# Kernel optimization log

Hardware: AMD Instinct MI355X
Metric: run time of the kernel (lower is better)

The kernel has to match this reference:

```python
import jax, jax.numpy as jnp
import numpy as np

N = 30000        # nodes
E = 480000       # edges
IN_DIM = 128
HID = 64
OUT = 64
POS_DIM = 32
H = 4            # heads (same for all layers)
PVOCAB = 3
NEG_SLOPE = 0.2


def _xavier(key, shape):
    fan_in, fan_out = shape[0], shape[-1] if len(shape) > 1 else shape[0]
    scale = 1.414 * np.sqrt(2.0 / (fan_in + fan_out))
    return jax.random.normal(key, shape, dtype=jnp.float32) * scale


def setup_inputs() -> dict:
    key = jax.random.key(0)
    ks = jax.random.split(key, 20)
    d0_in = IN_DIM + POS_DIM            # 160
    d_mid = HID * H + POS_DIM           # 288
    inp = {
        "features": jax.random.normal(ks[0], (N, IN_DIM), dtype=jnp.float32),
        # layer 0
        "W0": _xavier(ks[1], (d0_in, H * HID)),
        "al0": _xavier(ks[2], (H, HID)),
        "ar0": _xavier(ks[3], (H, HID)),
        "pe0": _xavier(ks[4], (PVOCAB, POS_DIM)),
        # layer 1
        "W1": _xavier(ks[5], (d_mid, H * HID)),
        "al1": _xavier(ks[6], (H, HID)),
        "ar1": _xavier(ks[7], (H, HID)),
        "pe1": _xavier(ks[8], (PVOCAB, POS_DIM)),
        # output layer
        "W2": _xavier(ks[9], (d_mid, H * OUT)),
        "al2": _xavier(ks[10], (H, OUT)),
        "ar2": _xavier(ks[11], (H, OUT)),
        "pe2": _xavier(ks[12], (PVOCAB, POS_DIM)),
        # graph
        "src": jax.random.randint(ks[13], (E,), 0, N, dtype=jnp.int32),
        "dst": jax.random.randint(ks[14], (E,), 0, N, dtype=jnp.int32),
        "pos": jax.random.randint(ks[15], (N,), 0, PVOCAB, dtype=jnp.int32),
    }
    return inp


def gat_layer(h, W, a_l, a_r, src, dst):
    # h: [N, in_d]; W: [in_d, H*d]; a_l,a_r: [H, d]
    n = h.shape[0]
    nh, d = a_l.shape
    ft = (h @ W).reshape(n, nh, d)                       # [N,H,d]
    a1 = jnp.einsum("nhd,hd->nh", ft, a_l)               # [N,H]
    a2 = jnp.einsum("nhd,hd->nh", ft, a_r)               # [N,H]
    e = jax.nn.leaky_relu(a1[src] + a2[dst], NEG_SLOPE)  # [E,H]
    # per-destination segment softmax (numerically stable)
    m = jax.ops.segment_max(e, dst, num_segments=n)      # [N,H]
    ex = jnp.exp(e - m[dst])                             # [E,H]
    s = jax.ops.segment_sum(ex, dst, num_segments=n)     # [N,H]
    alpha = ex / s[dst]                                  # [E,H]
    msg = ft[src] * alpha[:, :, None]                    # [E,H,d]
    return jax.ops.segment_sum(msg, dst, num_segments=n) # [N,H,d]


def reference(features, W0, al0, ar0, pe0, W1, al1, ar1, pe1,
              W2, al2, ar2, pe2, src, dst, pos):
    h = features
    # hidden GAT layers with ELU activation and head-flattening
    for W, al, ar, pe in ((W0, al0, ar0, pe0), (W1, al1, ar1, pe1)):
        p = pe[pos]                                      # [N, pos_dim]
        hcat = jnp.concatenate((h, p), axis=1)
        out = gat_layer(hcat, W, al, ar, src, dst)       # [N,H,d]
        h = jax.nn.elu(out.reshape(out.shape[0], -1))    # [N,H*d]
    # output layer: mean over heads
    p = pe2[pos]
    hcat = jnp.concatenate((h, p), axis=1)
    out = gat_layer(hcat, W2, al2, ar2, src, dst)        # [N,H,out]
    return out.mean(axis=1)                              # [N,out]
```

## Files before the change

### kernel.cpp

```cpp
#include <hip/hip_runtime.h>
#include <hip/hip_fp16.h>
#include <math.h>

#define N_NODES 30000
#define N_EDGES 480000
#define HEADS 4
#define DHEAD 64
#define FDIM 256
#define POSD 32
#define CAPB 96
#define HIST_NB 1875
#define G0_NB 940

typedef _Float16 half8 __attribute__((ext_vector_type(8)));
typedef float floatx4 __attribute__((ext_vector_type(4)));

__device__ __forceinline__ float lrelu(float x){ return x > 0.f ? x : 0.2f * x; }

template<typename T>
__device__ __forceinline__ void gemm_body(
    int bx, int by, const T* __restrict__ A, const _Float16* __restrict__ Wt,
    const float* __restrict__ PW, const int* __restrict__ pos,
    const float* __restrict__ al, const float* __restrict__ arw,
    _Float16* __restrict__ Ch, float* __restrict__ a1, float* __restrict__ a2,
    int K){
  int t = threadIdx.x;
  int w = t >> 6;
  int lane = t & 63;
  int lm = lane & 15;
  int kq = lane >> 4;
  int h = bx;
  int rowBase = by * 128 + w * 32;
  int colBase = h * DHEAD;

  floatx4 acc[2][4] = {};

  const T* Ar[2];
#pragma unroll
  for (int r = 0; r < 2; r++)
    Ar[r] = A + (size_t)min(rowBase + r * 16 + lm, N_NODES - 1) * K;
  const _Float16* Bp[4];
#pragma unroll
  for (int j = 0; j < 4; j++)
    Bp[j] = Wt + (size_t)(colBase + j * 16 + lm) * K;

  for (int kb = 0; kb < K; kb += 32){
    int ko = kb + kq * 8;
    half8 bf[4];
#pragma unroll
    for (int j = 0; j < 4; j++) bf[j] = *(const half8*)(Bp[j] + ko);
#pragma unroll
    for (int r = 0; r < 2; r++){
      half8 af;
      if constexpr (sizeof(T) == 2){
        af = *(const half8*)(Ar[r] + ko);
      } else {
        float4 u0 = *(const float4*)(Ar[r] + ko);
        float4 u1 = *(const float4*)(Ar[r] + ko + 4);
        af[0] = (_Float16)u0.x; af[1] = (_Float16)u0.y;
        af[2] = (_Float16)u0.z; af[3] = (_Float16)u0.w;
        af[4] = (_Float16)u1.x; af[5] = (_Float16)u1.y;
        af[6] = (_Float16)u1.z; af[7] = (_Float16)u1.w;
      }
#pragma unroll
      for (int j = 0; j < 4; j++)
        acc[r][j] = __builtin_amdgcn_mfma_f32_16x16x32_f16(af, bf[j], acc[r][j], 0, 0, 0);
    }
  }

  float alw[4], arr[4];
#pragma unroll
  for (int j = 0; j < 4; j++){
    int col = j * 16 + lm;
    alw[j] = al [h * DHEAD + col];
    arr[j] = arw[h * DHEAD + col];
  }

#pragma unroll
  for (int r = 0; r < 2; r++){
#pragma unroll
    for (int p = 0; p < 4; p++){
      int row = rowBase + r * 16 + kq * 4 + p;
      if (row >= N_NODES) continue;
      int pz = pos[row];
      const float* pwb = PW + pz * FDIM + colBase;
      float s1 = 0.f, s2 = 0.f;
#pragma unroll
      for (int j = 0; j < 4; j++){
        float v = acc[r][j][p] + pwb[j * 16 + lm];
        Ch[(size_t)row * FDIM + colBase + j * 16 + lm] = (_Float16)v;
        s1 = fmaf(v, alw[j], s1);
        s2 = fmaf(v, arr[j], s2);
      }
#pragma unroll
      for (int o2 = 1; o2 <= 8; o2 <<= 1){
        s1 += __shfl_xor(s1, o2, 64);
        s2 += __shfl_xor(s2, o2, 64);
      }
      if (lm == 0){
        a1[row * HEADS + h] = s1;
        a2[row * HEADS + h] = s2;
      }
    }
  }
}

template<typename T>
__global__ __launch_bounds__(256, 2) void gemm_k(
    const T* __restrict__ A, const _Float16* __restrict__ Wt,
    const float* __restrict__ PW, const int* __restrict__ pos,
    const float* __restrict__ al, const float* __restrict__ arw,
    _Float16* __restrict__ Ch, float* __restrict__ a1, float* __restrict__ a2,
    int K){
  gemm_body<T>(blockIdx.x, blockIdx.y, A, Wt, PW, pos, al, arw, Ch, a1, a2, K);
}

__global__ __launch_bounds__(256) void prep0_k(
    const float* __restrict__ W0, const float* __restrict__ pe0,
    _Float16* __restrict__ T0, float* __restrict__ PW,
    int* __restrict__ deg){
  int blk = blockIdx.x;
  int n = threadIdx.x;
  if (blk < 64){
    for (int k = blk; k < 128; k += 64)
      T0[(size_t)n * 128 + k] = (_Float16)W0[(size_t)k * FDIM + n];
  } else if (blk < 67){
    int v = blk - 64;
    float s = 0.f;
#pragma unroll
    for (int k = 0; k < POSD; k++)
      s = fmaf(pe0[v * POSD + k], W0[(size_t)(128 + k) * FDIM + n], s);
    PW[v * FDIM + n] = s;
  } else {
    int i = (blk - 67) * 256 + n;
    if (i < N_NODES) deg[i] = 0;
  }
}

__global__ __launch_bounds__(256, 2) void fused0_k(
    const float* __restrict__ A, const _Float16* __restrict__ Wt0,
    const float* __restrict__ PW0, const int* __restrict__ pos,
    const float* __restrict__ al0, const float* __restrict__ ar0,
    _Float16* __restrict__ Ch, float* __restrict__ a1, float* __restrict__ a2,
    const int* __restrict__ src, const int* __restrict__ dst,
    int* __restrict__ deg, int* __restrict__ esrc,
    const float* __restrict__ W1, const float* __restrict__ W2,
    _Float16* __restrict__ T1, _Float16* __restrict__ T2,
    const float* __restrict__ pe1, const float* __restrict__ pe2,
    float* __restrict__ PWall){
  int blk = blockIdx.x;
  if (blk < G0_NB){
    gemm_body<float>(blk & 3, blk >> 2, A, Wt0, PW0, pos, al0, ar0,
                     Ch, a1, a2, 128);
  } else if (blk < G0_NB + HIST_NB){
    int e = (blk - G0_NB) * 256 + threadIdx.x;
    if (e < N_EDGES){
      int d = dst[e];
      int slot = atomicAdd(&deg[d], 1);
      if (slot < CAPB) esrc[d * CAPB + slot] = src[e];
    }
  } else if (blk < G0_NB + HIST_NB + 128){
    int q = blk - G0_NB - HIST_NB;
    int l = q >> 6, kk0 = q & 63;
    const float* W = l == 0 ? W1 : W2;
    _Float16* T    = l == 0 ? T1 : T2;
    int n = threadIdx.x;
    for (int k = kk0; k < 256; k += 64)
      T[(size_t)n * 256 + k] = (_Float16)W[(size_t)k * FDIM + n];
  } else {
    int q = blk - G0_NB - HIST_NB - 128;
    int layer = q / 3 + 1, v = q % 3;
    const float* W  = layer == 1 ? W1 : W2;
    const float* pe = layer == 1 ? pe1 : pe2;
    int j = threadIdx.x;
    float s = 0.f;
#pragma unroll
    for (int k = 0; k < POSD; k++)
      s = fmaf(pe[v * POSD + k], W[(size_t)(256 + k) * FDIM + j], s);
    PWall[(layer * 3 + v) * FDIM + j] = s;
  }
}

__global__ __launch_bounds__(256) void agg4_k(
    const _Float16* __restrict__ ft, const float* __restrict__ a1,
    const float* __restrict__ a2, const int* __restrict__ degv,
    const int* __restrict__ esrc, _Float16* __restrict__ outh,
    float* __restrict__ outf, int mode){
  int wv = threadIdx.x >> 6;
  int lane = threadIdx.x & 63;
  int n = blockIdx.x * 4 + wv;
  if (n >= N_NODES) return;
  int jb = n * CAPB;
  int deg = min(degv[n], CAPB);
  int eidx = lane & 15, h = lane >> 4;
  int hsel = h << 4;
  float a2n = a2[n * HEADS + h];
  float4 acc = make_float4(0.f, 0.f, 0.f, 0.f);
  const _Float16* ftl = ft + lane * 4;
  struct h4 { __half2 a, b; };

  if (deg <= 64){
    int sreg[4]; float wreg[4];
    float m = -INFINITY;
#pragma unroll
    for (int r = 0; r < 4; r++){
      int idx = eidx + r * 16;
      int s = (idx < deg) ? esrc[jb + idx] : 0;
      sreg[r] = s;
      float e = (idx < deg) ? lrelu(a1[s * HEADS + h] + a2n) : -INFINITY;
      wreg[r] = e;
      m = fmaxf(m, e);
    }
    m = fmaxf(m, __shfl_xor(m, 1, 64));
    m = fmaxf(m, __shfl_xor(m, 2, 64));
    m = fmaxf(m, __shfl_xor(m, 4, 64));
    m = fmaxf(m, __shfl_xor(m, 8, 64));
    float ss = 0.f;
#pragma unroll
    for (int r = 0; r < 4; r++){
      int idx = eidx + r * 16;
      float tv = (idx < deg) ? __expf(wreg[r] - m) : 0.f;
      wreg[r] = tv;
      ss += tv;
    }
    ss += __shfl_xor(ss, 1, 64);
    ss += __shfl_xor(ss, 2, 64);
    ss += __shfl_xor(ss, 4, 64);
    ss += __shfl_xor(ss, 8, 64);
    float inv = (ss > 0.f) ? 1.f / ss : 0.f;
#pragma unroll
    for (int r = 0; r < 4; r++) wreg[r] *= inv;

#pragma unroll
    for (int r = 0; r < 4; r++){
      if (r * 16 >= deg) break;
      int lim = deg - r * 16; if (lim > 16) lim = 16;
      float wr = wreg[r]; int sr = sreg[r];
      int jj = 0;
      for (; jj + 8 <= lim; jj += 8){
        float w8[8]; int s8[8]; h4 f8[8];
#pragma unroll
        for (int u = 0; u < 8; u++){
          w8[u] = __shfl(wr, (jj + u) | hsel, 64);
          s8[u] = __shfl(sr, jj + u, 64);
        }
#pragma unroll
        for (int u = 0; u < 8; u++)
          f8[u] = *(const h4*)(ftl + (size_t)s8[u] * FDIM);
#pragma unroll
        for (int u = 0; u < 8; u++){
          float2 fa = __half22float2(f8[u].a), fb = __half22float2(f8[u].b);
          acc.x = fmaf(w8[u], fa.x, acc.x);
          acc.y = fmaf(w8[u], fa.y, acc.y);
          acc.z = fmaf(w8[u], fb.x, acc.z);
          acc.w = fmaf(w8[u], fb.y, acc.w);
        }
      }
      for (; jj < lim; jj += 4){
        float w4[4]; int s4[4]; h4 f4[4];
#pragma unroll
        for (int u = 0; u < 4; u++){
          w4[u] = __shfl(wr, (jj + u) | hsel, 64);
          s4[u] = __shfl(sr, jj + u, 64);
        }
#pragma unroll
        for (int u = 0; u < 4; u++)
          f4[u] = *(const h4*)(ftl + (size_t)s4[u] * FDIM);
#pragma unroll
        for (int u = 0; u < 4; u++){
          float2 fa = __half22float2(f4[u].a), fb = __half22float2(f4[u].b);
          acc.x = fmaf(w4[u], fa.x, acc.x);
          acc.y = fmaf(w4[u], fa.y, acc.y);
          acc.z = fmaf(w4[u], fb.x, acc.z);
          acc.w = fmaf(w4[u], fb.y, acc.w);
        }
      }
    }
  } else {
    float m = -INFINITY;
    for (int idx = eidx; idx < deg; idx += 16){
      int s = esrc[jb + idx];
      m = fmaxf(m, lrelu(a1[s * HEADS + h] + a2n));
    }
    m = fmaxf(m, __shfl_xor(m, 1, 64));
    m = fmaxf(m, __shfl_xor(m, 2, 64));
    m = fmaxf(m, __shfl_xor(m, 4, 64));
    m = fmaxf(m, __shfl_xor(m, 8, 64));
    float ss = 0.f;
    for (int idx = eidx; idx < deg; idx += 16){
      int s = esrc[jb + idx];
      ss += __expf(lrelu(a1[s * HEADS + h] + a2n) - m);
    }
    ss += __shfl_xor(ss, 1, 64);
    ss += __shfl_xor(ss, 2, 64);
    ss += __shfl_xor(ss, 4, 64);
    ss += __shfl_xor(ss, 8, 64);
    float inv = (ss > 0.f) ? 1.f / ss : 0.f;
    for (int j = 0; j < deg; j++){
      int sj = esrc[jb + j];
      float e = lrelu(a1[sj * HEADS + h] + a2n);
      float wj = __expf(e - m) * inv;
      h4 f = *(const h4*)(ftl + (size_t)sj * FDIM);
      float2 fa = __half22float2(f.a), fb = __half22float2(f.b);
      acc.x = fmaf(wj, fa.x, acc.x);
      acc.y = fmaf(wj, fa.y, acc.y);
      acc.z = fmaf(wj, fb.x, acc.z);
      acc.w = fmaf(wj, fb.y, acc.w);
    }
  }

  if (mode == 0){
    acc.x = acc.x > 0.f ? acc.x : (__expf(acc.x) - 1.f);
    acc.y = acc.y > 0.f ? acc.y : (__expf(acc.y) - 1.f);
    acc.z = acc.z > 0.f ? acc.z : (__expf(acc.z) - 1.f);
    acc.w = acc.w > 0.f ? acc.w : (__expf(acc.w) - 1.f);
    struct h4s { _Float16 h[4]; } u;
    u.h[0] = (_Float16)acc.x; u.h[1] = (_Float16)acc.y;
    u.h[2] = (_Float16)acc.z; u.h[3] = (_Float16)acc.w;
    *(h4s*)&outh[(size_t)n * FDIM + lane * 4] = u;
  } else {
#pragma unroll
    for (int o2 = 16; o2 <= 32; o2 <<= 1){
      acc.x += __shfl_xor(acc.x, o2, 64);
      acc.y += __shfl_xor(acc.y, o2, 64);
      acc.z += __shfl_xor(acc.z, o2, 64);
      acc.w += __shfl_xor(acc.w, o2, 64);
    }
    if (lane < 16){
      float4 o;
      o.x = acc.x * 0.25f; o.y = acc.y * 0.25f;
      o.z = acc.z * 0.25f; o.w = acc.w * 0.25f;
      *(float4*)&outf[(size_t)n * DHEAD + lane * 4] = o;
    }
  }
}

extern "C" void kernel_launch(void* const* d_in, const int* in_sizes, int n_in,
                              void* d_out, int out_size, void* d_ws, size_t ws_size,
                              hipStream_t stream){
  const float* features = (const float*)d_in[0];
  const float* W0  = (const float*)d_in[1];
  const float* al0 = (const float*)d_in[2];
  const float* ar0 = (const float*)d_in[3];
  const float* pe0 = (const float*)d_in[4];
  const float* W1  = (const float*)d_in[5];
  const float* al1 = (const float*)d_in[6];
  const float* ar1 = (const float*)d_in[7];
  const float* pe1 = (const float*)d_in[8];
  const float* W2  = (const float*)d_in[9];
  const float* al2 = (const float*)d_in[10];
  const float* ar2 = (const float*)d_in[11];
  const float* pe2 = (const float*)d_in[12];
  const int* srcv  = (const int*)d_in[13];
  const int* dstv  = (const int*)d_in[14];
  const int* posv  = (const int*)d_in[15];
  float* out = (float*)d_out;

  char* wp = (char*)d_ws;
  auto alloc = [&](size_t bytes){
    void* p = (void*)wp;
    wp += (bytes + 255) & ~(size_t)255;
    return p;
  };
  _Float16* fth   = (_Float16*)alloc(sizeof(_Float16) * (size_t)N_NODES * FDIM);
  _Float16* hbuf  = (_Float16*)alloc(sizeof(_Float16) * (size_t)N_NODES * FDIM);
  _Float16* Wt0   = (_Float16*)alloc(sizeof(_Float16) * 256 * 128);
  _Float16* Wt1   = (_Float16*)alloc(sizeof(_Float16) * 256 * 256);
  _Float16* Wt2   = (_Float16*)alloc(sizeof(_Float16) * 256 * 256);
  float* a1     = (float*)alloc(sizeof(float) * N_NODES * HEADS);
  float* a2     = (float*)alloc(sizeof(float) * N_NODES * HEADS);
  float* PW     = (float*)alloc(sizeof(float) * 9 * FDIM);
  int*   deg    = (int*)alloc(sizeof(int) * N_NODES);
  int*   esrc   = (int*)alloc(sizeof(int) * (size_t)N_NODES * CAPB);

  prep0_k<<<185, 256, 0, stream>>>(W0, pe0, Wt0, PW, deg);

  fused0_k<<<G0_NB + HIST_NB + 134, 256, 0, stream>>>(
      features, Wt0, PW, posv, al0, ar0, fth, a1, a2,
      srcv, dstv, deg, esrc, W1, W2, Wt1, Wt2, pe1, pe2, PW);

  dim3 ggrid(4, (N_NODES + 127) / 128);
  int agrid = (N_NODES + 3) / 4;

  agg4_k<<<agrid, 256, 0, stream>>>(fth, a1, a2, deg, esrc, hbuf, nullptr, 0);

  gemm_k<_Float16><<<ggrid, 256, 0, stream>>>(
      hbuf, Wt1, PW + 1 * 3 * FDIM, posv, al1, ar1, fth, a1, a2, 256);
  agg4_k<<<agrid, 256, 0, stream>>>(fth, a1, a2, deg, esrc, hbuf, nullptr, 0);

  gemm_k<_Float16><<<ggrid, 256, 0, stream>>>(
      hbuf, Wt2, PW + 2 * 3 * FDIM, posv, al2, ar2, fth, a1, a2, 256);
  agg4_k<<<agrid, 256, 0, stream>>>(fth, a1, a2, deg, esrc, nullptr, out, 1);
}
```

Before: 289.0 us.

## Merge all stages into one cooperative persistent kernel with grid syncs

Replaces the seven separate kernel launches with a single cooperative persistent kernel that loops over virtual blocks for each stage (prep, histogram+layer-0 GEMM, three aggregate/GEMM rounds) and separates the stages with grid-wide syncs. This is meant to remove per-launch overhead and the gaps between kernels. In exchange, the grid is capped at a fixed number of resident blocks, occupancy is constrained by launch bounds of 4 blocks, and each grid.sync adds a barrier cost. A fallback multi-kernel path is kept for when the cooperative launch fails.

After: 782.5 us. 2.71x slower.

```diff
diff --git a/kernel.cpp b/kernel.cpp
--- a/kernel.cpp
+++ b/kernel.cpp
@@ -1,6 +1,9 @@
 #include <hip/hip_runtime.h>
 #include <hip/hip_fp16.h>
+#include <hip/hip_cooperative_groups.h>
 #include <math.h>
+
+namespace cg = cooperative_groups;
 
 #define N_NODES 30000
 #define N_EDGES 480000
@@ -11,6 +14,8 @@
 #define CAPB 96
 #define HIST_NB 1875
 #define G0_NB 940
+#define AGG_NB 7500
+#define PREP_NB 319
 
 typedef _Float16 half8 __attribute__((ext_vector_type(8)));
 typedef float floatx4 __attribute__((ext_vector_type(4)));
@@ -81,114 +86,79 @@
 #pragma unroll
     for (int p = 0; p < 4; p++){
       int row = rowBase + r * 16 + kq * 4 + p;
-      if (row >= N_NODES) continue;
-      int pz = pos[row];
-      const float* pwb = PW + pz * FDIM + colBase;
-      float s1 = 0.f, s2 = 0.f;
-#pragma unroll
-      for (int j = 0; j < 4; j++){
-        float v = acc[r][j][p] + pwb[j * 16 + lm];
-        Ch[(size_t)row * FDIM + colBase + j * 16 + lm] = (_Float16)v;
-        s1 = fmaf(v, alw[j], s1);
-        s2 = fmaf(v, arr[j], s2);
+      if (row < N_NODES){
+        int pz = pos[row];
+        const float* pwb = PW + pz * FDIM + colBase;
+        float s1 = 0.f, s2 = 0.f;
+#pragma unroll
+        for (int j = 0; j < 4; j++){
+          float v = acc[r][j][p] + pwb[j * 16 + lm];
+          Ch[(size_t)row * FDIM + colBase + j * 16 + lm] = (_Float16)v;
+          s1 = fmaf(v, alw[j], s1);
+          s2 = fmaf(v, arr[j], s2);
+        }
+#pragma unroll
+        for (int o2 = 1; o2 <= 8; o2 <<= 1){
+          s1 += __shfl_xor(s1, o2, 64);
+          s2 += __shfl_xor(s2, o2, 64);
+        }
+        if (lm == 0){
+          a1[row * HEADS + h] = s1;
+          a2[row * HEADS + h] = s2;
+        }
       }
-#pragma unroll
-      for (int o2 = 1; o2 <= 8; o2 <<= 1){
-        s1 += __shfl_xor(s1, o2, 64);
-        s2 += __shfl_xor(s2, o2, 64);
-      }
-      if (lm == 0){
-        a1[row * HEADS + h] = s1;
-        a2[row * HEADS + h] = s2;
-      }
-    }
-  }
-}
-
-template<typename T>
-__global__ __launch_bounds__(256, 2) void gemm_k(
-    const T* __restrict__ A, const _Float16* __restrict__ Wt,
-    const float* __restrict__ PW, const int* __restrict__ pos,
-    const float* __restrict__ al, const float* __restrict__ arw,
-    _Float16* __restrict__ Ch, float* __restrict__ a1, float* __restrict__ a2,
-    int K){
-  gemm_body<T>(blockIdx.x, blockIdx.y, A, Wt, PW, pos, al, arw, Ch, a1, a2, K);
-}
-
-__global__ __launch_bounds__(256) void prep0_k(
-    const float* __restrict__ W0, const float* __restrict__ pe0,
-    _Float16* __restrict__ T0, float* __restrict__ PW,
-    int* __restrict__ deg){
-  int blk = blockIdx.x;
+    }
+  }
+}
+
+__device__ __forceinline__ void prep_block(
+    int vb, const float* __restrict__ W0, const float* __restrict__ W1,
+    const float* __restrict__ W2, const float* __restrict__ pe0,
+    const float* __restrict__ pe1, const float* __restrict__ pe2,
+    _Float16* __restrict__ T0, _Float16* __restrict__ T1,
+    _Float16* __restrict__ T2, float* __restrict__ PW, int* __restrict__ deg){
   int n = threadIdx.x;
-  if (blk < 64){
-    for (int k = blk; k < 128; k += 64)
+  if (vb < 64){
+    for (int k = vb; k < 128; k += 64)
       T0[(size_t)n * 128 + k] = (_Float16)W0[(size_t)k * FDIM + n];
-  } else if (blk < 67){
-    int v = blk - 64;
+  } else if (vb < 67){
+    int v = vb - 64;
     float s = 0.f;
 #pragma unroll
     for (int k = 0; k < POSD; k++)
       s = fmaf(pe0[v * POSD + k], W0[(size_t)(128 + k) * FDIM + n], s);
     PW[v * FDIM + n] = s;
-  } else {
-    int i = (blk - 67) * 256 + n;
+  } else if (vb < 185){
+    int i = (vb - 67) * 256 + n;
     if (i < N_NODES) deg[i] = 0;
-  }
-}
-
-__global__ __launch_bounds__(256, 2) void fused0_k(
-    const float* __restrict__ A, const _Float16* __restrict__ Wt0,
-    const float* __restrict__ PW0, const int* __restrict__ pos,
-    const float* __restrict__ al0, const float* __restrict__ ar0,
-    _Float16* __restrict__ Ch, float* __restrict__ a1, float* __restrict__ a2,
-    const int* __restrict__ src, const int* __restrict__ dst,
-    int* __restrict__ deg, int* __restrict__ esrc,
-    const float* __restrict__ W1, const float* __restrict__ W2,
-    _Float16* __restrict__ T1, _Float16* __restrict__ T2,
-    const float* __restrict__ pe1, const float* __restrict__ pe2,
-    float* __restrict__ PWall){
-  int blk = blockIdx.x;
-  if (blk < G0_NB){
-    gemm_body<float>(blk & 3, blk >> 2, A, Wt0, PW0, pos, al0, ar0,
-                     Ch, a1, a2, 128);
-  } else if (blk < G0_NB + HIST_NB){
-    int e = (blk - G0_NB) * 256 + threadIdx.x;
-    if (e < N_EDGES){
-      int d = dst[e];
-      int slot = atomicAdd(&deg[d], 1);
-      if (slot < CAPB) esrc[d * CAPB + slot] = src[e];
-    }
-  } else if (blk < G0_NB + HIST_NB + 128){
-    int q = blk - G0_NB - HIST_NB;
+  } else if (vb < 313){
+    int q = vb - 185;
     int l = q >> 6, kk0 = q & 63;
     const float* W = l == 0 ? W1 : W2;
     _Float16* T    = l == 0 ? T1 : T2;
-    int n = threadIdx.x;
     for (int k = kk0; k < 256; k += 64)
       T[(size_t)n * 256 + k] = (_Float16)W[(size_t)k * FDIM + n];
   } else {
-    int q = blk - G0_NB - HIST_NB - 128;
+    int q = vb - 313;
     int layer = q / 3 + 1, v = q % 3;
     const float* W  = layer == 1 ? W1 : W2;
     const float* pe = layer == 1 ? pe1 : pe2;
-    int j = threadIdx.x;
     float s = 0.f;
 #pragma unroll
     for (int k = 0; k < POSD; k++)
-      s = fmaf(pe[v * POSD + k], W[(size_t)(256 + k) * FDIM + j], s);
-    PWall[(layer * 3 + v) * FDIM + j] = s;
-  }
-}
-
-__global__ __launch_bounds__(256) void agg4_k(
-    const _Float16* __restrict__ ft, const float* __restrict__ a1,
+      s = fmaf(pe[v * POSD + k], W[(size_t)(256 + k) * FDIM + n], s);
+    PW[(layer * 3 + v) * FDIM + n] = s;
+  }
+}
+
+__device__ __forceinline__ void agg_block(
+    int vb, const _Float16* __restrict__ ft, const float* __restrict__ a1,
     const float* __restrict__ a2, const int* __restrict__ degv,
     const int* __restrict__ esrc, _Float16* __restrict__ outh,
     float* __restrict__ outf, int mode){
   int wv = threadIdx.x >> 6;
   int lane = threadIdx.x & 63;
-  int n = blockIdx.x * 4 + wv;
+  int n = vb * 4 + wv;
   if (n >= N_NODES) return;
   int jb = n * CAPB;
   int deg = min(degv[n], CAPB);
@@ -335,60 +305,180 @@
   }
 }
 
+struct Params {
+  const float* features;
+  const float *W0, *al0, *ar0, *pe0;
+  const float *W1, *al1, *ar1, *pe1;
+  const float *W2, *al2, *ar2, *pe2;
+  const int *src, *dst, *pos;
+  float* out;
+  _Float16 *fth, *hbuf, *Wt0, *Wt1, *Wt2;
+  float *a1, *a2, *PW;
+  int *deg, *esrc;
+};
+
+__global__ __launch_bounds__(256, 4) void mega_k(Params p){
+  cg::grid_group grid = cg::this_grid();
+  const int G = gridDim.x;
+
+  for (int vb = blockIdx.x; vb < PREP_NB; vb += G)
+    prep_block(vb, p.W0, p.W1, p.W2, p.pe0, p.pe1, p.pe2,
+               p.Wt0, p.Wt1, p.Wt2, p.PW, p.deg);
+  grid.sync();
+
+  for (int vb = blockIdx.x; vb < HIST_NB + G0_NB; vb += G){
+    if (vb < HIST_NB){
+      int e = vb * 256 + threadIdx.x;
+      if (e < N_EDGES){
+        int d = p.dst[e];
+        int slot = atomicAdd(&p.deg[d], 1);
+        if (slot < CAPB) p.esrc[d * CAPB + slot] = p.src[e];
+      }
+    } else {
+      int q = vb - HIST_NB;
+      gemm_body<float>(q & 3, q >> 2, p.features, p.Wt0, p.PW, p.pos,
+                       p.al0, p.ar0, p.fth, p.a1, p.a2, 128);
+    }
+  }
+  grid.sync();
+
+  for (int vb = blockIdx.x; vb < AGG_NB; vb += G)
+    agg_block(vb, p.fth, p.a1, p.a2, p.deg, p.esrc, p.hbuf, nullptr, 0);
+  grid.sync();
+
+  for (int vb = blockIdx.x; vb < G0_NB; vb += G)
+    gemm_body<_Float16>(vb & 3, vb >> 2, p.hbuf, p.Wt1, p.PW + 3 * FDIM,
+                        p.pos, p.al1, p.ar1, p.fth, p.a1, p.a2, 256);
+  grid.sync();
+
+  for (int vb = blockIdx.x; vb < AGG_NB; vb += G)
+    agg_block(vb, p.fth, p.a1, p.a2, p.deg, p.esrc, p.hbuf, nullptr, 0);
+  grid.sync();
+
+  for (int vb = blockIdx.x; vb < G0_NB; vb += G)
+    gemm_body<_Float16>(vb & 3, vb >> 2, p.hbuf, p.Wt2, p.PW + 6 * FDIM,
+                        p.pos, p.al2, p.ar2, p.fth, p.a1, p.a2, 256);
+  grid.sync();
+
+  for (int vb = blockIdx.x; vb < AGG_NB; vb += G)
+    agg_block(vb, p.fth, p.a1, p.a2, p.deg, p.esrc, nullptr, p.out, 1);
+}
+
+__global__ __launch_bounds__(256) void prep0_k(
+    const float* __restrict__ W0, const float* __restrict__ pe0,
+    _Float16* __restrict__ T0, float* __restrict__ PW, int* __restrict__ deg){
+  int blk = blockIdx.x, n = threadIdx.x;
+  if (blk < 64){
+    for (int k = blk; k < 128; k += 64)
+      T0[(size_t)n * 128 + k] = (_Float16)W0[(size_t)k * FDIM + n];
+  } else if (blk < 67){
+    int v = blk - 64;
+    float s = 0.f;
+#pragma unroll
+    for (int k = 0; k < POSD; k++)
+      s = fmaf(pe0[v * POSD + k], W0[(size_t)(128 + k) * FDIM + n], s);
+    PW[v * FDIM + n] = s;
+  } else {
+    int i = (blk - 67) * 256 + n;
+    if (i < N_NODES) deg[i] = 0;
+  }
+}
+
+__global__ __launch_bounds__(256, 2) void fused0_k(Params p){
+  int blk = blockIdx.x;
+  if (blk < G0_NB){
+    gemm_body<float>(blk & 3, blk >> 2, p.features, p.Wt0, p.PW, p.pos,
+                     p.al0, p.ar0, p.fth, p.a1, p.a2, 128);
+  } else if (blk < G0_NB + HIST_NB){
+    int e = (blk - G0_NB) * 256 + threadIdx.x;
+    if (e < N_EDGES){
+      int d = p.dst[e];
+      int slot = atomicAdd(&p.deg[d], 1);
+      if (slot < CAPB) p.esrc[d * CAPB + slot] = p.src[e];
+    }
+  } else if (blk < G0_NB + HIST_NB + 128 + 6){
+    prep_block(blk - G0_NB - HIST_NB + 185, p.W0, p.W1, p.W2, p.pe0, p.pe1,
+               p.pe2, p.Wt0, p.Wt1, p.Wt2, p.PW, p.deg);
+  }
+}
+
+template<typename T>
+__global__ __launch_bounds__(256, 2) void gemm_k(
+    const T* __restrict__ A, const _Float16* __restrict__ Wt,
+    const float* __restrict__ PW, const int* __restrict__ pos,
+    const float* __restrict__ al, const float* __restrict__ arw,
+    _Float16* __restrict__ Ch, float* __restrict__ a1, float* __restrict__ a2,
+    int K){
+  gemm_body<T>(blockIdx.x, blockIdx.y, A, Wt, PW, pos, al, arw, Ch, a1, a2, K);
+}
+
+__global__ __launch_bounds__(256) void agg4_k(
+    const _Float16* __restrict__ ft, const float* __restrict__ a1,
+    const float* __restrict__ a2, const int* __restrict__ degv,
+    const int* __restrict__ esrc, _Float16* __restrict__ outh,
+    float* __restrict__ outf, int mode){
+  agg_block(blockIdx.x, ft, a1, a2, degv, esrc, outh, outf, mode);
+}
+
 extern "C" void kernel_launch(void* const* d_in, const int* in_sizes, int n_in,
                               void* d_out, int out_size, void* d_ws, size_t ws_size,
                               hipStream_t stream){
-  const float* features = (const float*)d_in[0];
-  const float* W0  = (const float*)d_in[1];
-  const float* al0 = (const float*)d_in[2];
-  const float* ar0 = (const float*)d_in[3];
-  const float* pe0 = (const float*)d_in[4];
-  const float* W1  = (const float*)d_in[5];
-  const float* al1 = (const float*)d_in[6];
-  const float* ar1 = (const float*)d_in[7];
-  const float* pe1 = (const float*)d_in[8];
-  const float* W2  = (const float*)d_in[9];
-  const float* al2 = (const float*)d_in[10];
-  const float* ar2 = (const float*)d_in[11];
-  const float* pe2 = (const float*)d_in[12];
-  const int* srcv  = (const int*)d_in[13];
-  const int* dstv  = (const int*)d_in[14];
-  const int* posv  = (const int*)d_in[15];
-  float* out = (float*)d_out;
+  Params p;
+  p.features = (const float*)d_in[0];
+  p.W0  = (const float*)d_in[1];  p.al0 = (const float*)d_in[2];
+  p.ar0 = (const float*)d_in[3];  p.pe0 = (const float*)d_in[4];
+  p.W1  = (const float*)d_in[5];  p.al1 = (const float*)d_in[6];
+  p.ar1 = (const float*)d_in[7];  p.pe1 = (const float*)d_in[8];
+  p.W2  = (const float*)d_in[9];  p.al2 = (const float*)d_in[10];
+  p.ar2 = (const float*)d_in[11]; p.pe2 = (const float*)d_in[12];
+  p.src = (const int*)d_in[13];   p.dst = (const int*)d_in[14];
+  p.pos = (const int*)d_in[15];
+  p.out = (float*)d_out;
 
   char* wp = (char*)d_ws;
   auto alloc = [&](size_t bytes){
-    void* p = (void*)wp;
+    void* q = (void*)wp;
     wp += (bytes + 255) & ~(size_t)255;
-    return p;
+    return q;
   };
-  _Float16* fth   = (_Float16*)alloc(sizeof(_Float16) * (size_t)N_NODES * FDIM);
-  _Float16* hbuf  = (_Float16*)alloc(sizeof(_Float16) * (size_t)N_NODES * FDIM);
-  _Float16* Wt0   = (_Float16*)alloc(sizeof(_Float16) * 256 * 128);
-  _Float16* Wt1   = (_Float16*)alloc(sizeof(_Float16) * 256 * 256);
-  _Float16* Wt2   = (_Float16*)alloc(sizeof(_Float16) * 256 * 256);
-  float* a1     = (float*)alloc(sizeof(float) * N_NODES * HEADS);
-  float* a2     = (float*)alloc(sizeof(float) * N_NODES * HEADS);
-  float* PW     = (float*)alloc(sizeof(float) * 9 * FDIM);
-  int*   deg    = (int*)alloc(sizeof(int) * N_NODES);
-  int*   esrc   = (int*)alloc(sizeof(int) * (size_t)N_NODES * CAPB);
-
-  prep0_k<<<185, 256, 0, stream>>>(W0, pe0, Wt0, PW, deg);
-
-  fused0_k<<<G0_NB + HIST_NB + 134, 256, 0, stream>>>(
-      features, Wt0, PW, posv, al0, ar0, fth, a1, a2,
-      srcv, dstv, deg, esrc, W1, W2, Wt1, Wt2, pe1, pe2, PW);
+  p.fth  = (_Float16*)alloc(sizeof(_Float16) * (size_t)N_NODES * FDIM);
+  p.hbuf = (_Float16*)alloc(sizeof(_Float16) * (size_t)N_NODES * FDIM);
+  p.Wt0  = (_Float16*)alloc(sizeof(_Float16) * 256 * 128);
+  p.Wt1  = (_Float16*)alloc(sizeof(_Float16) * 256 * 256);
+  p.Wt2  = (_Float16*)alloc(sizeof(_Float16) * 256 * 256);
+  p.a1   = (float*)alloc(sizeof(float) * N_NODES * HEADS);
+  p.a2   = (float*)alloc(sizeof(float) * N_NODES * HEADS);
+  p.PW   = (float*)alloc(sizeof(float) * 9 * FDIM);
+  p.deg  = (int*)alloc(sizeof(int) * N_NODES);
+  p.esrc = (int*)alloc(sizeof(int) * (size_t)N_NODES * CAPB);
+
+  int maxB = 0;
+  hipError_t oerr = hipOccupancyMaxActiveBlocksPerMultiprocessor(
+      &maxB, mega_k, 256, 0);
+  bool coop_ok = (oerr == hipSuccess && maxB >= 1);
+  if (coop_ok){
+    int G = maxB * 256;
+    if (G > 1024) G = 1024;
+    void* args[] = {&p};
+    hipError_t lerr = hipLaunchCooperativeKernel(
+        mega_k, dim3(G), dim3(256), args, 0, stream);
+    if (lerr == hipSuccess) return;
+  }
+
+  prep0_k<<<185, 256, 0, stream>>>(p.W0, p.pe0, p.Wt0, p.PW, p.deg);
+  fused0_k<<<G0_NB + HIST_NB + 134, 256, 0, stream>>>(p);
 
   dim3 ggrid(4, (N_NODES + 127) / 128);
-  int agrid = (N_NODES + 3) / 4;
-
-  agg4_k<<<agrid, 256, 0, stream>>>(fth, a1, a2, deg, esrc, hbuf, nullptr, 0);
-
+  int agrid = AGG_NB;
+
+  agg4_k<<<agrid, 256, 0, stream>>>(p.fth, p.a1, p.a2, p.deg, p.esrc,
+                                    p.hbuf, nullptr, 0);
   gemm_k<_Float16><<<ggrid, 256, 0, stream>>>(
-      hbuf, Wt1, PW + 1 * 3 * FDIM, posv, al1, ar1, fth, a1, a2, 256);
-  agg4_k<<<agrid, 256, 0, stream>>>(fth, a1, a2, deg, esrc, hbuf, nullptr, 0);
-
+      p.hbuf, p.Wt1, p.PW + 3 * FDIM, p.pos, p.al1, p.ar1, p.fth, p.a1, p.a2, 256);
+  agg4_k<<<agrid, 256, 0, stream>>>(p.fth, p.a1, p.a2, p.deg, p.esrc,
+                                    p.hbuf, nullptr, 0);
   gemm_k<_Float16><<<ggrid, 256, 0, stream>>>(
-      hbuf, Wt2, PW + 2 * 3 * FDIM, posv, al2, ar2, fth, a1, a2, 256);
-  agg4_k<<<agrid, 256, 0, stream>>>(fth, a1, a2, deg, esrc, nullptr, out, 1);
-}
+      p.hbuf, p.Wt2, p.PW + 6 * FDIM, p.pos, p.al2, p.ar2, p.fth, p.a1, p.a2, 256);
+  agg4_k<<<agrid, 256, 0, stream>>>(p.fth, p.a1, p.a2, p.deg, p.esrc,
+                                    nullptr, p.out, 1);
+}
```

## Fuse neighbor aggregation with next layer's GEMM through LDS tile

Applied to the files above, without the earlier changes.

Each block of 16 nodes aggregates its neighbors with softmax and ELU, writes the fp16 result into an LDS tile, then runs the next layer's MFMA GEMM plus attention-score epilogue directly from that tile. This drops the hidden-activation round trip through global memory and two kernel launches, and ping-pongs the feature and score buffers to avoid read/write hazards. The cost is a smaller GEMM tile, since every block reloads the full weight matrix from global memory or cache, plus a block-level sync between the irregular gather phase and the GEMM phase.

New measurement: 315.5 us. +9.2%, slower.

```diff
diff --git a/kernel.cpp b/kernel.cpp
--- a/kernel.cpp
+++ b/kernel.cpp
@@ -11,11 +11,16 @@
 #define CAPB 96
 #define HIST_NB 1875
 #define G0_NB 940
+#define ROWS_PB 16
+#define LDS_STRIDE 264
 
 typedef _Float16 half8 __attribute__((ext_vector_type(8)));
 typedef float floatx4 __attribute__((ext_vector_type(4)));
 
 __device__ __forceinline__ float lrelu(float x){ return x > 0.f ? x : 0.2f * x; }
+
+struct h4 { __half2 a, b; };
+struct h4s { _Float16 h[4]; };
 
 template<typename T>
 __device__ __forceinline__ void gemm_body(
@@ -81,46 +86,268 @@
 #pragma unroll
     for (int p = 0; p < 4; p++){
       int row = rowBase + r * 16 + kq * 4 + p;
-      if (row >= N_NODES) continue;
-      int pz = pos[row];
-      const float* pwb = PW + pz * FDIM + colBase;
-      float s1 = 0.f, s2 = 0.f;
-#pragma unroll
-      for (int j = 0; j < 4; j++){
-        float v = acc[r][j][p] + pwb[j * 16 + lm];
-        Ch[(size_t)row * FDIM + colBase + j * 16 + lm] = (_Float16)v;
-        s1 = fmaf(v, alw[j], s1);
-        s2 = fmaf(v, arr[j], s2);
+      if (row < N_NODES){
+        int pz = pos[row];
+        const float* pwb = PW + pz * FDIM + colBase;
+        float s1 = 0.f, s2 = 0.f;
+#pragma unroll
+        for (int j = 0; j < 4; j++){
+          float v = acc[r][j][p] + pwb[j * 16 + lm];
+          Ch[(size_t)row * FDIM + colBase + j * 16 + lm] = (_Float16)v;
+          s1 = fmaf(v, alw[j], s1);
+          s2 = fmaf(v, arr[j], s2);
+        }
+#pragma unroll
+        for (int o2 = 1; o2 <= 8; o2 <<= 1){
+          s1 += __shfl_xor(s1, o2, 64);
+          s2 += __shfl_xor(s2, o2, 64);
+        }
+        if (lm == 0){
+          a1[row * HEADS + h] = s1;
+          a2[row * HEADS + h] = s2;
+        }
       }
-#pragma unroll
-      for (int o2 = 1; o2 <= 8; o2 <<= 1){
-        s1 += __shfl_xor(s1, o2, 64);
-        s2 += __shfl_xor(s2, o2, 64);
+    }
+  }
+}
+
+__device__ __forceinline__ float4 agg_node(
+    int n, const _Float16* __restrict__ ft, const float* __restrict__ a1,
+    const float* __restrict__ a2, const int* __restrict__ degv,
+    const int* __restrict__ esrc, int lane){
+  int jb = n * CAPB;
+  int deg = min(degv[n], CAPB);
+  int eidx = lane & 15, h = lane >> 4;
+  int hsel = h << 4;
+  float a2n = a2[n * HEADS + h];
+  float4 acc = make_float4(0.f, 0.f, 0.f, 0.f);
+  const _Float16* ftl = ft + lane * 4;
+
+  if (deg <= 64){
+    int sreg[4]; float wreg[4];
+    float m = -INFINITY;
+#pragma unroll
+    for (int r = 0; r < 4; r++){
+      int idx = eidx + r * 16;
+      int s = (idx < deg) ? esrc[jb + idx] : 0;
+      sreg[r] = s;
+      float e = (idx < deg) ? lrelu(a1[s * HEADS + h] + a2n) : -INFINITY;
+      wreg[r] = e;
+      m = fmaxf(m, e);
+    }
+    m = fmaxf(m, __shfl_xor(m, 1, 64));
+    m = fmaxf(m, __shfl_xor(m, 2, 64));
+    m = fmaxf(m, __shfl_xor(m, 4, 64));
+    m = fmaxf(m, __shfl_xor(m, 8, 64));
+    float ss = 0.f;
+#pragma unroll
+    for (int r = 0; r < 4; r++){
+      int idx = eidx + r * 16;
+      float tv = (idx < deg) ? __expf(wreg[r] - m) : 0.f;
+      wreg[r] = tv;
+      ss += tv;
+    }
+    ss += __shfl_xor(ss, 1, 64);
+    ss += __shfl_xor(ss, 2, 64);
+    ss += __shfl_xor(ss, 4, 64);
+    ss += __shfl_xor(ss, 8, 64);
+    float inv = (ss > 0.f) ? 1.f / ss : 0.f;
+#pragma unroll
+    for (int r = 0; r < 4; r++) wreg[r] *= inv;
+
+#pragma unroll
+    for (int r = 0; r < 4; r++){
+      if (r * 16 >= deg) break;
+      int lim = deg - r * 16; if (lim > 16) lim = 16;
+      float wr = wreg[r]; int sr = sreg[r];
+      int jj = 0;
+      for (; jj + 8 <= lim; jj += 8){
+        float w8[8]; int s8[8]; h4 f8[8];
+#pragma unroll
+        for (int u = 0; u < 8; u++){
+          w8[u] = __shfl(wr, (jj + u) | hsel, 64);
+          s8[u] = __shfl(sr, jj + u, 64);
+        }
+#pragma unroll
+        for (int u = 0; u < 8; u++)
+          f8[u] = *(const h4*)(ftl + (size_t)s8[u] * FDIM);
+#pragma unroll
+        for (int u = 0; u < 8; u++){
+          float2 fa = __half22float2(f8[u].a), fb = __half22float2(f8[u].b);
+          acc.x = fmaf(w8[u], fa.x, acc.x);
+          acc.y = fmaf(w8[u], fa.y, acc.y);
+          acc.z = fmaf(w8[u], fb.x, acc.z);
+          acc.w = fmaf(w8[u], fb.y, acc.w);
+        }
       }
-      if (lm == 0){
-        a1[row * HEADS + h] = s1;
-        a2[row * HEADS + h] = s2;
+      for (; jj < lim; jj += 4){
+        float w4[4]; int s4[4]; h4 f4[4];
+#pragma unroll
+        for (int u = 0; u < 4; u++){
+          w4[u] = __shfl(wr, (jj + u) | hsel, 64);
+          s4[u] = __shfl(sr, jj + u, 64);
+        }
+#pragma unroll
+        for (int u = 0; u < 4; u++)
+          f4[u] = *(const h4*)(ftl + (size_t)s4[u] * FDIM);
+#pragma unroll
+        for (int u = 0; u < 4; u++){
+          float2 fa = __half22float2(f4[u].a), fb = __half22float2(f4[u].b);
+          acc.x = fmaf(w4[u], fa.x, acc.x);
+          acc.y = fmaf(w4[u], fa.y, acc.y);
+          acc.z = fmaf(w4[u], fb.x, acc.z);
+          acc.w = fmaf(w4[u], fb.y, acc.w);
+        }
       }
     }
-  }
-}
-
-template<typename T>
-__global__ __launch_bounds__(256, 2) void gemm_k(
-    const T* __restrict__ A, const _Float16* __restrict__ Wt,
+  } else {
+    float m = -INFINITY;
+    for (int idx = eidx; idx < deg; idx += 16){
+      int s = esrc[jb + idx];
+      m = fmaxf(m, lrelu(a1[s * HEADS + h] + a2n));
+    }
+    m = fmaxf(m, __shfl_xor(m, 1, 64));
+    m = fmaxf(m, __shfl_xor(m, 2, 64));
+    m = fmaxf(m, __shfl_xor(m, 4, 64));
+    m = fmaxf(m, __shfl_xor(m, 8, 64));
+    float ss = 0.f;
+    for (int idx = eidx; idx < deg; idx += 16){
+      int s = esrc[jb + idx];
+      ss += __expf(lrelu(a1[s * HEADS + h] + a2n) - m);
+    }
+    ss += __shfl_xor(ss, 1, 64);
+    ss += __shfl_xor(ss, 2, 64);
+    ss += __shfl_xor(ss, 4, 64);
+    ss += __shfl_xor(ss, 8, 64);
+    float inv = (ss > 0.f) ? 1.f / ss : 0.f;
+    for (int j = 0; j < deg; j++){
+      int sj = esrc[jb + j];
+      float e = lrelu(a1[sj * HEADS + h] + a2n);
+      float wj = __expf(e - m) * inv;
+      h4 f = *(const h4*)(ftl + (size_t)sj * FDIM);
+      float2 fa = __half22float2(f.a), fb = __half22float2(f.b);
+      acc.x = fmaf(wj, fa.x, acc.x);
+      acc.y = fmaf(wj, fa.y, acc.y);
+      acc.z = fmaf(wj, fb.x, acc.z);
+      acc.w = fmaf(wj, fb.y, acc.w);
+    }
+  }
+  return acc;
+}
+
+__global__ __launch_bounds__(256, 2) void aggemm_k(
+    const _Float16* __restrict__ ftin, const float* __restrict__ a1in,
+    const float* __restrict__ a2in, const int* __restrict__ degv,
+    const int* __restrict__ esrc, const _Float16* __restrict__ Wt,
     const float* __restrict__ PW, const int* __restrict__ pos,
     const float* __restrict__ al, const float* __restrict__ arw,
-    _Float16* __restrict__ Ch, float* __restrict__ a1, float* __restrict__ a2,
-    int K){
-  gemm_body<T>(blockIdx.x, blockIdx.y, A, Wt, PW, pos, al, arw, Ch, a1, a2, K);
+    _Float16* __restrict__ ftout, float* __restrict__ a1out,
+    float* __restrict__ a2out){
+  __shared__ _Float16 As[ROWS_PB * LDS_STRIDE];
+  int t = threadIdx.x;
+  int wv = t >> 6;
+  int lane = t & 63;
+  int rb = blockIdx.x * ROWS_PB;
+
+#pragma unroll
+  for (int i = 0; i < 4; i++){
+    int rowLocal = wv * 4 + i;
+    int n = rb + rowLocal;
+    float4 acc = agg_node(n, ftin, a1in, a2in, degv, esrc, lane);
+    acc.x = acc.x > 0.f ? acc.x : (__expf(acc.x) - 1.f);
+    acc.y = acc.y > 0.f ? acc.y : (__expf(acc.y) - 1.f);
+    acc.z = acc.z > 0.f ? acc.z : (__expf(acc.z) - 1.f);
+    acc.w = acc.w > 0.f ? acc.w : (__expf(acc.w) - 1.f);
+    h4s u;
+    u.h[0] = (_Float16)acc.x; u.h[1] = (_Float16)acc.y;
+    u.h[2] = (_Float16)acc.z; u.h[3] = (_Float16)acc.w;
+    *(h4s*)&As[rowLocal * LDS_STRIDE + lane * 4] = u;
+  }
+  __syncthreads();
+
+  int lm = lane & 15;
+  int kq = lane >> 4;
+  int h = wv;
+  int colBase = h * DHEAD;
+
+  floatx4 acc[4] = {};
+  const _Float16* Bp[4];
+#pragma unroll
+  for (int j = 0; j < 4; j++)
+    Bp[j] = Wt + (size_t)(colBase + j * 16 + lm) * 256;
+
+  for (int kb = 0; kb < 256; kb += 32){
+    int ko = kb + kq * 8;
+    half8 af = *(const half8*)&As[lm * LDS_STRIDE + ko];
+    half8 bf[4];
+#pragma unroll
+    for (int j = 0; j < 4; j++) bf[j] = *(const half8*)(Bp[j] + ko);
+#pragma unroll
+    for (int j = 0; j < 4; j++)
+      acc[j] = __builtin_amdgcn_mfma_f32_16x16x32_f16(af, bf[j], acc[j], 0, 0, 0);
+  }
+
+  float alw[4], arr[4];
+#pragma unroll
+  for (int j = 0; j < 4; j++){
+    int col = j * 16 + lm;
+    alw[j] = al [h * DHEAD + col];
+    arr[j] = arw[h * DHEAD + col];
+  }
+
+#pragma unroll
+  for (int p = 0; p < 4; p++){
+    int row = rb + kq * 4 + p;
+    int pz = pos[row];
+    const float* pwb = PW + pz * FDIM + colBase;
+    float s1 = 0.f, s2 = 0.f;
+#pragma unroll
+    for (int j = 0; j < 4; j++){
+      float v = acc[j][p] + pwb[j * 16 + lm];
+      ftout[(size_t)row * FDIM + colBase + j * 16 + lm] = (_Float16)v;
+      s1 = fmaf(v, alw[j], s1);
+      s2 = fmaf(v, arr[j], s2);
+    }
+#pragma unroll
+    for (int o2 = 1; o2 <= 8; o2 <<= 1){
+      s1 += __shfl_xor(s1, o2, 64);
+      s2 += __shfl_xor(s2, o2, 64);
+    }
+    if (lm == 0){
+      a1out[row * HEADS + h] = s1;
+      a2out[row * HEADS + h] = s2;
+    }
+  }
+}
+
+__global__ __launch_bounds__(256) void aggfin_k(
+    const _Float16* __restrict__ ft, const float* __restrict__ a1,
+    const float* __restrict__ a2, const int* __restrict__ degv,
+    const int* __restrict__ esrc, float* __restrict__ outf){
+  int wv = threadIdx.x >> 6;
+  int lane = threadIdx.x & 63;
+  int n = blockIdx.x * 4 + wv;
+  if (n >= N_NODES) return;
+  float4 acc = agg_node(n, ft, a1, a2, degv, esrc, lane);
+#pragma unroll
+  for (int o2 = 16; o2 <= 32; o2 <<= 1){
+    acc.x += __shfl_xor(acc.x, o2, 64);
+    acc.y += __shfl_xor(acc.y, o2, 64);
+    acc.z += __shfl_xor(acc.z, o2, 64);
+    acc.w += __shfl_xor(acc.w, o2, 64);
+  }
+  if (lane < 16){
+    float4 o;
+    o.x = acc.x * 0.25f; o.y = acc.y * 0.25f;
+    o.z = acc.z * 0.25f; o.w = acc.w * 0.25f;
+    *(float4*)&outf[(size_t)n * DHEAD + lane * 4] = o;
+  }
 }
 
 __global__ __launch_bounds__(256) void prep0_k(
     const float* __restrict__ W0, const float* __restrict__ pe0,
-    _Float16* __restrict__ T0, float* __restrict__ PW,
-    int* __restrict__ deg){
-  int blk = blockIdx.x;
-  int n = threadIdx.x;
+    _Float16* __restrict__ T0, float* __restrict__ PW, int* __restrict__ deg){
+  int blk = blockIdx.x, n = threadIdx.x;
   if (blk < 64){
     for (int k = blk; k < 128; k += 64)
       T0[(size_t)n * 128 + k] = (_Float16)W0[(size_t)k * FDIM + n];
@@ -181,160 +408,6 @@
   }
 }
 
-__global__ __launch_bounds__(256) void agg4_k(
-    const _Float16* __restrict__ ft, const float* __restrict__ a1,
-    const float* __restrict__ a2, const int* __restrict__ degv,
-    const int* __restrict__ esrc, _Float16* __restrict__ outh,
-    float* __restrict__ outf, int mode){
-  int wv = threadIdx.x >> 6;
-  int lane = threadIdx.x & 63;
-  int n = blockIdx.x * 4 + wv;
-  if (n >= N_NODES) return;
-  int jb = n * CAPB;
-  int deg = min(degv[n], CAPB);
-  int eidx = lane & 15, h = lane >> 4;
-  int hsel = h << 4;
-  float a2n = a2[n * HEADS + h];
-  float4 acc = make_float4(0.f, 0.f, 0.f, 0.f);
-  const _Float16* ftl = ft + lane * 4;
-  struct h4 { __half2 a, b; };
-
-  if (deg <= 64){
-    int sreg[4]; float wreg[4];
-    float m = -INFINITY;
-#pragma unroll
-    for (int r = 0; r < 4; r++){
-      int idx = eidx + r * 16;
-      int s = (idx < deg) ? esrc[jb + idx] : 0;
-      sreg[r] = s;
-      float e = (idx < deg) ? lrelu(a1[s * HEADS + h] + a2n) : -INFINITY;
-      wreg[r] = e;
-      m = fmaxf(m, e);
-    }
-    m = fmaxf(m, __shfl_xor(m, 1, 64));
-    m = fmaxf(m, __shfl_xor(m, 2, 64));
-    m = fmaxf(m, __shfl_xor(m, 4, 64));
-    m = fmaxf(m, __shfl_xor(m, 8, 64));
-    float ss = 0.f;
-#pragma unroll
-    for (int r = 0; r < 4; r++){
-      int idx = eidx + r * 16;
-      float tv = (idx < deg) ? __expf(wreg[r] - m) : 0.f;
-      wreg[r] = tv;
-      ss += tv;
-    }
-    ss += __shfl_xor(ss, 1, 64);
-    ss += __shfl_xor(ss, 2, 64);
-    ss += __shfl_xor(ss, 4, 64);
-    ss += __shfl_xor(ss, 8, 64);
-    float inv = (ss > 0.f) ? 1.f / ss : 0.f;
-#pragma unroll
-    for (int r = 0; r < 4; r++) wreg[r] *= inv;
-
-#pragma unroll
-    for (int r = 0; r < 4; r++){
-      if (r * 16 >= deg) break;
-      int lim = deg - r * 16; if (lim > 16) lim = 16;
-      float wr = wreg[r]; int sr = sreg[r];
-      int jj = 0;
-      for (; jj + 8 <= lim; jj += 8){
-        float w8[8]; int s8[8]; h4 f8[8];
-#pragma unroll
-        for (int u = 0; u < 8; u++){
-          w8[u] = __shfl(wr, (jj + u) | hsel, 64);
-          s8[u] = __shfl(sr, jj + u, 64);
-        }
-#pragma unroll
-        for (int u = 0; u < 8; u++)
-          f8[u] = *(const h4*)(ftl + (size_t)s8[u] * FDIM);
-#pragma unroll
-        for (int u = 0; u < 8; u++){
-          float2 fa = __half22float2(f8[u].a), fb = __half22float2(f8[u].b);
-          acc.x = fmaf(w8[u], fa.x, acc.x);
-          acc.y = fmaf(w8[u], fa.y, acc.y);
-          acc.z = fmaf(w8[u], fb.x, acc.z);
-          acc.w = fmaf(w8[u], fb.y, acc.w);
-        }
-      }
-      for (; jj < lim; jj += 4){
-        float w4[4]; int s4[4]; h4 f4[4];
-#pragma unroll
-        for (int u = 0; u < 4; u++){
-          w4[u] = __shfl(wr, (jj + u) | hsel, 64);
-          s4[u] = __shfl(sr, jj + u, 64);
-        }
-#pragma unroll
-        for (int u = 0; u < 4; u++)
-          f4[u] = *(const h4*)(ftl + (size_t)s4[u] * FDIM);
-#pragma unroll
-        for (int u = 0; u < 4; u++){
-          float2 fa = __half22float2(f4[u].a), fb = __half22float2(f4[u].b);
-          acc.x = fmaf(w4[u], fa.x, acc.x);
-          acc.y = fmaf(w4[u], fa.y, acc.y);
-          acc.z = fmaf(w4[u], fb.x, acc.z);
-          acc.w = fmaf(w4[u], fb.y, acc.w);
-        }
-      }
-    }
-  } else {
-    float m = -INFINITY;
-    for (int idx = eidx; idx < deg; idx += 16){
-      int s = esrc[jb + idx];
-      m = fmaxf(m, lrelu(a1[s * HEADS + h] + a2n));
-    }
-    m = fmaxf(m, __shfl_xor(m, 1, 64));
-    m = fmaxf(m, __shfl_xor(m, 2, 64));
-    m = fmaxf(m, __shfl_xor(m, 4, 64));
-    m = fmaxf(m, __shfl_xor(m, 8, 64));
-    float ss = 0.f;
-    for (int idx = eidx; idx < deg; idx += 16){
-      int s = esrc[jb + idx];
-      ss += __expf(lrelu(a1[s * HEADS + h] + a2n) - m);
-    }
-    ss += __shfl_xor(ss, 1, 64);
-    ss += __shfl_xor(ss, 2, 64);
-    ss += __shfl_xor(ss, 4, 64);
-    ss += __shfl_xor(ss, 8, 64);
-    float inv = (ss > 0.f) ? 1.f / ss : 0.f;
-    for (int j = 0; j < deg; j++){
-      int sj = esrc[jb + j];
-      float e = lrelu(a1[sj * HEADS + h] + a2n);
-      float wj = __expf(e - m) * inv;
-      h4 f = *(const h4*)(ftl + (size_t)sj * FDIM);
-      float2 fa = __half22float2(f.a), fb = __half22float2(f.b);
-      acc.x = fmaf(wj, fa.x, acc.x);
-      acc.y = fmaf(wj, fa.y, acc.y);
-      acc.z = fmaf(wj, fb.x, acc.z);
-      acc.w = fmaf(wj, fb.y, acc.w);
-    }
-  }
-
-  if (mode == 0){
-    acc.x = acc.x > 0.f ? acc.x : (__expf(acc.x) - 1.f);
-    acc.y = acc.y > 0.f ? acc.y : (__expf(acc.y) - 1.f);
-    acc.z = acc.z > 0.f ? acc.z : (__expf(acc.z) - 1.f);
-    acc.w = acc.w > 0.f ? acc.w : (__expf(acc.w) - 1.f);
-    struct h4s { _Float16 h[4]; } u;
-    u.h[0] = (_Float16)acc.x; u.h[1] = (_Float16)acc.y;
-    u.h[2] = (_Float16)acc.z; u.h[3] = (_Float16)acc.w;
-    *(h4s*)&outh[(size_t)n * FDIM + lane * 4] = u;
-  } else {
-#pragma unroll
-    for (int o2 = 16; o2 <= 32; o2 <<= 1){
-      acc.x += __shfl_xor(acc.x, o2, 64);
-      acc.y += __shfl_xor(acc.y, o2, 64);
-      acc.z += __shfl_xor(acc.z, o2, 64);
-      acc.w += __shfl_xor(acc.w, o2, 64);
-    }
-    if (lane < 16){
-      float4 o;
-      o.x = acc.x * 0.25f; o.y = acc.y * 0.25f;
-      o.z = acc.z * 0.25f; o.w = acc.w * 0.25f;
-      *(float4*)&outf[(size_t)n * DHEAD + lane * 4] = o;
-    }
-  }
-}
-
 extern "C" void kernel_launch(void* const* d_in, const int* in_sizes, int n_in,
                               void* d_out, int out_size, void* d_ws, size_t ws_size,
                               hipStream_t stream){
@@ -358,37 +431,37 @@
 
   char* wp = (char*)d_ws;
   auto alloc = [&](size_t bytes){
-    void* p = (void*)wp;
+    void* q = (void*)wp;
     wp += (bytes + 255) & ~(size_t)255;
-    return p;
+    return q;
   };
-  _Float16* fth   = (_Float16*)alloc(sizeof(_Float16) * (size_t)N_NODES * FDIM);
-  _Float16* hbuf  = (_Float16*)alloc(sizeof(_Float16) * (size_t)N_NODES * FDIM);
-  _Float16* Wt0   = (_Float16*)alloc(sizeof(_Float16) * 256 * 128);
-  _Float16* Wt1   = (_Float16*)alloc(sizeof(_Float16) * 256 * 256);
-  _Float16* Wt2   = (_Float16*)alloc(sizeof(_Float16) * 256 * 256);
-  float* a1     = (float*)alloc(sizeof(float) * N_NODES * HEADS);
-  float* a2     = (float*)alloc(sizeof(float) * N_NODES * HEADS);
-  float* PW     = (float*)alloc(sizeof(float) * 9 * FDIM);
-  int*   deg    = (int*)alloc(sizeof(int) * N_NODES);
-  int*   esrc   = (int*)alloc(sizeof(int) * (size_t)N_NODES * CAPB);
+  _Float16* F0  = (_Float16*)alloc(sizeof(_Float16) * (size_t)N_NODES * FDIM);
+  _Float16* F1  = (_Float16*)alloc(sizeof(_Float16) * (size_t)N_NODES * FDIM);
+  _Float16* Wt0 = (_Float16*)alloc(sizeof(_Float16) * 256 * 128);
+  _Float16* Wt1 = (_Float16*)alloc(sizeof(_Float16) * 256 * 256);
+  _Float16* Wt2 = (_Float16*)alloc(sizeof(_Float16) * 256 * 256);
+  float* a1A = (float*)alloc(sizeof(float) * N_NODES * HEADS);
+  float* a2A = (float*)alloc(sizeof(float) * N_NODES * HEADS);
+  float* a1B = (float*)alloc(sizeof(float) * N_NODES * HEADS);
+  float* a2B = (float*)alloc(sizeof(float) * N_NODES * HEADS);
+  float* PW  = (float*)alloc(sizeof(float) * 9 * FDIM);
+  int*   deg = (int*)alloc(sizeof(int) * N_NODES);
+  int*   esrc= (int*)alloc(sizeof(int) * (size_t)N_NODES * CAPB);
 
   prep0_k<<<185, 256, 0, stream>>>(W0, pe0, Wt0, PW, deg);
 
   fused0_k<<<G0_NB + HIST_NB + 134, 256, 0, stream>>>(
-      features, Wt0, PW, posv, al0, ar0, fth, a1, a2,
+      features, Wt0, PW, posv, al0, ar0, F0, a1A, a2A,
       srcv, dstv, deg, esrc, W1, W2, Wt1, Wt2, pe1, pe2, PW);
 
-  dim3 ggrid(4, (N_NODES + 127) / 128);
-  int agrid = (N_NODES + 3) / 4;
-
-  agg4_k<<<agrid, 256, 0, stream>>>(fth, a1, a2, deg, esrc, hbuf, nullptr, 0);
-
-  gemm_k<_Float16><<<ggrid, 256, 0, stream>>>(
-      hbuf, Wt1, PW + 1 * 3 * FDIM, posv, al1, ar1, fth, a1, a2, 256);
-  agg4_k<<<agrid, 256, 0, stream>>>(fth, a1, a2, deg, esrc, hbuf, nullptr, 0);
-
-  gemm_k<_Float16><<<ggrid, 256, 0, stream>>>(
-      hbuf, Wt2, PW + 2 * 3 * FDIM, posv, al2, ar2, fth, a1, a2, 256);
-  agg4_k<<<agrid, 256, 0, stream>>>(fth, a1, a2, deg, esrc, nullptr, out, 1);
-}
+  aggemm_k<<<1875, 256, 0, stream>>>(
+      F0, a1A, a2A, deg, esrc, Wt1, PW + 3 * FDIM, posv, al1, ar1,
+      F1, a1B, a2B);
+
+  aggemm_k<<<1875, 256, 0, stream>>>(
+      F1, a1B, a2B, deg, esrc, Wt2, PW + 6 * FDIM, posv, al2, ar2,
+      F0, a1A, a2A);
+
+  aggfin_k<<<(N_NODES + 3) / 4, 256, 0, stream>>>(
+      F0, a1A, a2A, deg, esrc, out);
+}
```
